# Performance work log

Measured on AMD Instinct MI355X. Metric: run time of the kernel, lower is better.

The kernel has to match this reference:

```python
import jax, jax.numpy as jnp
import numpy as np

B, N, D, K = 8, 2048, 512, 8192
DECAY = 0.99
COMMIT = 0.25
EPS = 1e-5


def setup_inputs() -> dict:
    key = jax.random.key(0)
    k1, k2 = jax.random.split(key, 2)
    encoded_latents = jax.random.normal(k1, (B, N, D), dtype=jnp.float32)
    embedding_weight = jax.random.normal(k2, (K, D), dtype=jnp.float32)
    # buffers: ema_codebook initialized as a clone of the embedding, sizes at zero
    ema_cluster_sizes = jnp.zeros((K,), dtype=jnp.float32)
    ema_codebook = embedding_weight
    return {
        "encoded_latents": encoded_latents,
        "embedding_weight": embedding_weight,
        "ema_cluster_sizes": ema_cluster_sizes,
        "ema_codebook": ema_codebook,
    }


def reference(encoded_latents, embedding_weight, ema_cluster_sizes, ema_codebook):
    # (B, N, D) -> (B*N, D)
    z = encoded_latents.reshape(-1, D)
    e = embedding_weight

    # ||z - e||^2 = z^2 - 2 z.e + e^2  via matmul  -> (B*N, K)
    z_sq = jnp.sum(z * z, axis=1, keepdims=True)
    e_sq = jnp.sum(e * e, axis=1)
    distances = z_sq - 2.0 * (z @ e.T) + e_sq

    nearest = jnp.argmin(distances, axis=-1)          # (B*N,)
    quantized_flat = e[nearest]                        # gather -> (B*N, D)

    # --- training-mode EMA codebook update (no-grad buffer math) ---
    z_ng = jax.lax.stop_gradient(z)
    cluster_sizes = jax.ops.segment_sum(
        jnp.ones(z.shape[0], dtype=jnp.float32), nearest, num_segments=K)
    weighted_sum = jax.ops.segment_sum(z_ng, nearest, num_segments=K)
    new_ema_cluster_sizes = ema_cluster_sizes * DECAY + cluster_sizes * (1.0 - DECAY)
    new_ema_codebook = ema_codebook * DECAY + weighted_sum * (1.0 - DECAY)
    new_embedding = new_ema_codebook / (new_ema_cluster_sizes[:, None] + EPS)

    quantized = quantized_flat.reshape(B, N, D)
    commitment_loss = COMMIT * jnp.mean(
        (encoded_latents - jax.lax.stop_gradient(quantized)) ** 2)

    # STE exactly as written in the torch module: grad flows into `quantized`
    quantized_ste = quantized + jax.lax.stop_gradient(encoded_latents - quantized)
    indices = nearest.reshape(B, N)
    return (quantized_ste, indices, commitment_loss,
            new_ema_cluster_sizes, new_ema_codebook, new_embedding)
```

## Files before the change

kernel.cpp:

```cpp
#include <hip/hip_runtime.h>
#include <cfloat>

#define B_SZ 8
#define N_SZ 2048
#define D_SZ 512
#define K_SZ 8192
#define M_SZ (B_SZ * N_SZ)

#define DECAY_F 0.99f
#define OMD_F ((float)(1.0 - 0.99))
#define EPS_F 1e-5f

#define OUT1_OFF 8388608
#define OUT2_OFF 8404992
#define OUT3_OFF 8404993
#define OUT4_OFF 8413185
#define OUT5_OFF 12607489

typedef unsigned short ushort_t;
typedef unsigned int uint_t;
typedef short bf16x8 __attribute__((ext_vector_type(8)));
typedef float f32x4 __attribute__((ext_vector_type(4)));

__device__ inline ushort_t f2bf(float v) {
    union { float f; uint_t u; } x; x.f = v;
    uint_t r = x.u + 0x7FFFu + ((x.u >> 16) & 1u);
    return (ushort_t)(r >> 16);
}

__device__ __forceinline__ void gl16(const void* g, void* l) {
    __builtin_amdgcn_global_load_lds(
        (const __attribute__((address_space(1))) uint_t*)g,
        (__attribute__((address_space(3))) uint_t*)l, 16, 0, 0);
}

__global__ __launch_bounds__(256) void k_esq(const float* __restrict__ e,
                                             float* __restrict__ esq) {
    int row = blockIdx.x * 4 + (threadIdx.x >> 6);
    int lane = threadIdx.x & 63;
    const float4* er = (const float4*)(e + (size_t)row * D_SZ);
    float s = 0.f;
#pragma unroll
    for (int i = 0; i < 2; ++i) {
        float4 v = er[lane + i * 64];
        s += v.x * v.x + v.y * v.y + v.z * v.z + v.w * v.w;
    }
#pragma unroll
    for (int off = 32; off; off >>= 1) s += __shfl_down(s, off);
    if (lane == 0) esq[row] = s;
}

__global__ __launch_bounds__(256) void k_split_e(const float* __restrict__ in,
                                                 ushort_t* __restrict__ ebuf) {
    int idx = blockIdx.x * 256 + threadIdx.x;
    int row = idx >> 6, o = idx & 63;
    int ch = o >> 3, kg = o & 7;
    const float* src = in + (size_t)row * D_SZ + o * 8;
    float4 a = *(const float4*)src;
    float4 b = *(const float4*)(src + 4);
    float vv[8] = {a.x, a.y, a.z, a.w, b.x, b.y, b.z, b.w};
    ushort_t o1[8];
#pragma unroll
    for (int j = 0; j < 8; ++j) o1[j] = f2bf(vv[j]);
    int cb = row >> 7, rl = row & 127;
    size_t base = (size_t)(cb * 8 + ch) * 16384 + rl * 128;
    *(uint4*)((unsigned char*)ebuf + base + ((kg ^ (rl & 7)) << 4)) = *(uint4*)o1;
}

__global__ __launch_bounds__(256) void k_split_z(const float* __restrict__ in,
                                                 ushort_t* __restrict__ zbuf) {
    int idx = blockIdx.x * 256 + threadIdx.x;
    int row = idx >> 6, o = idx & 63;
    int ch = o >> 3, kg = o & 7;
    const float* src = in + (size_t)row * D_SZ + o * 8;
    float4 a = *(const float4*)src;
    float4 b = *(const float4*)(src + 4);
    float vv[8] = {a.x, a.y, a.z, a.w, b.x, b.y, b.z, b.w};
    ushort_t o1[8];
#pragma unroll
    for (int j = 0; j < 8; ++j) o1[j] = f2bf(vv[j]);
    int zi = row >> 7, rl = row & 127;
    size_t base = (size_t)(zi * 8 + ch) * 16384 + rl * 128;
    *(uint4*)((unsigned char*)zbuf + base + ((kg ^ (rl & 7)) << 4)) = *(uint4*)o1;
}

__global__ __launch_bounds__(256) void k_init(const float* __restrict__ cb,
                                              const float* __restrict__ sizes,
                                              float* __restrict__ out3,
                                              float* __restrict__ out4) {
    int i = blockIdx.x * 256 + threadIdx.x;
    out4[i] = cb[i] * DECAY_F;
    if (i < K_SZ) out3[i] = sizes[i] * DECAY_F;
}

__global__ __launch_bounds__(256) void k_copy(const float* __restrict__ z,
                                              float* __restrict__ out0) {
    int i = blockIdx.x * 256 + threadIdx.x;
    ((float4*)out0)[i] = ((const float4*)z)[i];
}

__global__ __launch_bounds__(256) void k_scatter(const float* __restrict__ z,
                                                 const float* __restrict__ e,
                                                 const int* __restrict__ nearest,
                                                 float* __restrict__ out3,
                                                 float* __restrict__ out4,
                                                 float* __restrict__ lossAcc) {
    const int tid = threadIdx.x;
    float lp = 0.f;
    const int base_row = blockIdx.x * 8;
#pragma unroll
    for (int r = 0; r < 8; ++r) {
        int row = base_row + r;
        int n = nearest[row];
        float2 zv = ((const float2*)(z + (size_t)row * D_SZ))[tid];
        float2 ev = ((const float2*)(e + (size_t)n * D_SZ))[tid];
        float* o4 = out4 + (size_t)n * D_SZ + tid * 2;
        atomicAdd(o4, OMD_F * zv.x);
        atomicAdd(o4 + 1, OMD_F * zv.y);
        float dx = zv.x - ev.x, dy = zv.y - ev.y;
        lp += dx * dx + dy * dy;
        if (tid == 0) atomicAdd(out3 + n, OMD_F);
    }
#pragma unroll
    for (int off = 32; off; off >>= 1) lp += __shfl_down(lp, off);
    __shared__ float red[4];
    if ((tid & 63) == 0) red[tid >> 6] = lp;
    __syncthreads();
    if (tid == 0) atomicAdd(lossAcc, red[0] + red[1] + red[2] + red[3]);
}

__global__ __launch_bounds__(256) void k_final(const float* __restrict__ out3,
                                               const float* __restrict__ out4,
                                               float* __restrict__ out5,
                                               const float* __restrict__ lossAcc,
                                               float* __restrict__ out2) {
    int i = blockIdx.x * 256 + threadIdx.x;
    out5[i] = out4[i] / (out3[i >> 9] + EPS_F);
    if (i == 0) out2[0] = 0.25f * lossAcc[0] / 8388608.0f;
}

__global__ __launch_bounds__(512, 4) void k_pass1(const ushort_t* __restrict__ ebuf,
                                                  const ushort_t* __restrict__ zbuf,
                                                  const float* __restrict__ esq,
                                                  float* __restrict__ candD,
                                                  ushort_t* __restrict__ candI) {
    __shared__ __align__(16) unsigned char ldsb[65536];

    const int tid = threadIdx.x;
    const int lane = tid & 63;
    const int wv = tid >> 6;
    const int mw = wv >> 2;
    const int nw = wv & 3;
    const int lr = lane & 15;
    const int g = lane >> 4;

    const int xcd = blockIdx.x & 7;
    const int cbl = (blockIdx.x >> 3) & 7;
    const int zi = blockIdx.x >> 6;
    const int cb = xcd * 8 + cbl;

    const unsigned char* esrc = (const unsigned char*)ebuf + (size_t)cb * 131072 + tid * 16;
    const unsigned char* zsrc = (const unsigned char*)zbuf + (size_t)zi * 131072 + tid * 16;

#define ISSUE(c, b) do {                                                \
        const unsigned char* ep_ = esrc + (c) * 16384;                  \
        const unsigned char* zp_ = zsrc + (c) * 16384;                  \
        unsigned char* el_ = ldsb + (b) * 32768 + tid * 16;             \
        unsigned char* zl_ = el_ + 16384;                               \
        gl16(ep_, el_); gl16(ep_ + 8192, el_ + 8192);                   \
        gl16(zp_, zl_); gl16(zp_ + 8192, zl_ + 8192);                   \
    } while (0)

    f32x4 acc[4][2];
#pragma unroll
    for (int mf = 0; mf < 4; ++mf)
#pragma unroll
        for (int nf = 0; nf < 2; ++nf)
            acc[mf][nf] = (f32x4){0.f, 0.f, 0.f, 0.f};

    ISSUE(0, 0);
    asm volatile("s_waitcnt vmcnt(0)" ::: "memory");
    __builtin_amdgcn_s_barrier();
    asm volatile("" ::: "memory");

    int cur = 0;
    for (int ch = 0; ch < 8; ++ch) {
        if (ch < 7) {
            if (cur) ISSUE(ch + 1, 0); else ISSUE(ch + 1, 1);
        }

        const unsigned char* eb = ldsb + cur * 32768;
        const unsigned char* zp = eb + 16384;

#pragma unroll
        for (int ks = 0; ks < 2; ++ks) {
            bf16x8 zf[2];
#pragma unroll
            for (int nf = 0; nf < 2; ++nf) {
                int row = nw * 32 + nf * 16 + lr;
                int sl = (ks * 4 + g) ^ (row & 7);
                zf[nf] = *(const bf16x8*)(zp + row * 128 + (sl << 4));
            }
#pragma unroll
            for (int mf = 0; mf < 4; ++mf) {
                int row = mw * 64 + mf * 16 + lr;
                int sl = (ks * 4 + g) ^ (row & 7);
                bf16x8 ef = *(const bf16x8*)(eb + row * 128 + (sl << 4));
#pragma unroll
                for (int nf = 0; nf < 2; ++nf)
                    acc[mf][nf] = __builtin_amdgcn_mfma_f32_16x16x32_bf16(ef, zf[nf], acc[mf][nf], 0, 0, 0);
            }
        }
        asm volatile("s_waitcnt vmcnt(0)" ::: "memory");
        __builtin_amdgcn_s_barrier();
        asm volatile("" ::: "memory");
        cur ^= 1;
    }
#undef ISSUE

    float b1[2], b2[2];
    int i1[2], i2[2];
#pragma unroll
    for (int nf = 0; nf < 2; ++nf) {
        b1[nf] = FLT_MAX; b2[nf] = FLT_MAX;
        i1[nf] = 0x7fffffff; i2[nf] = 0x7fffffff;
    }
    const int code0 = cb * 128 + mw * 64;
#pragma unroll
    for (int mf = 0; mf < 4; ++mf)
#pragma unroll
        for (int r = 0; r < 4; ++r) {
            int code = code0 + mf * 16 + g * 4 + r;
            float eq = esq[code];
#pragma unroll
            for (int nf = 0; nf < 2; ++nf) {
                float d = fmaf(-2.f, acc[mf][nf][r], eq);
                if (d < b1[nf]) {
                    b2[nf] = b1[nf]; i2[nf] = i1[nf];
                    b1[nf] = d; i1[nf] = code;
                } else if (d < b2[nf]) {
                    b2[nf] = d; i2[nf] = code;
                }
            }
        }

#pragma unroll
    for (int off = 16; off <= 32; off <<= 1) {
#pragma unroll
        for (int nf = 0; nf < 2; ++nf) {
            float ob1 = __shfl_xor(b1[nf], off); int oi1 = __shfl_xor(i1[nf], off);
            float ob2 = __shfl_xor(b2[nf], off); int oi2 = __shfl_xor(i2[nf], off);
            bool tA = (b1[nf] < ob1) || (b1[nf] == ob1 && i1[nf] <= oi1);
            float n1 = tA ? b1[nf] : ob1; int ni1 = tA ? i1[nf] : oi1;
            float ca = tA ? b2[nf] : ob2; int cia = tA ? i2[nf] : oi2;
            float cbv = tA ? ob1 : b1[nf]; int cib = tA ? oi1 : i1[nf];
            bool t2 = (ca < cbv) || (ca == cbv && cia <= cib);
            b1[nf] = n1; i1[nf] = ni1;
            b2[nf] = t2 ? ca : cbv; i2[nf] = t2 ? cia : cib;
        }
    }

    __syncthreads();
    float* mD = (float*)ldsb;
    int* mI = (int*)(ldsb + 1024);
    if (mw == 1 && g == 0) {
#pragma unroll
        for (int nf = 0; nf < 2; ++nf) {
            int zr = nw * 32 + nf * 16 + lr;
            mD[zr * 2] = b1[nf]; mD[zr * 2 + 1] = b2[nf];
            mI[zr * 2] = i1[nf]; mI[zr * 2 + 1] = i2[nf];
        }
    }
    __syncthreads();
    if (mw == 0 && g == 0) {
#pragma unroll
        for (int nf = 0; nf < 2; ++nf) {
            int zr = nw * 32 + nf * 16 + lr;
            float ob1 = mD[zr * 2], ob2 = mD[zr * 2 + 1];
            int oi1 = mI[zr * 2], oi2 = mI[zr * 2 + 1];
            bool tA = (b1[nf] < ob1) || (b1[nf] == ob1 && i1[nf] <= oi1);
            float n1 = tA ? b1[nf] : ob1; int ni1 = tA ? i1[nf] : oi1;
            float ca = tA ? b2[nf] : ob2; int cia = tA ? i2[nf] : oi2;
            float cbv = tA ? ob1 : b1[nf]; int cib = tA ? oi1 : i1[nf];
            bool t2 = (ca < cbv) || (ca == cbv && cia <= cib);
            float n2 = t2 ? ca : cbv; int ni2 = t2 ? cia : cib;
            int row = zi * 128 + zr;
            size_t base = (size_t)row * 128 + cb * 2;
            candD[base] = n1; candD[base + 1] = n2;
            candI[base] = (ushort_t)ni1; candI[base + 1] = (ushort_t)ni2;
        }
    }
}

__global__ __launch_bounds__(256) void k_refine(const float* __restrict__ z,
                                                const float* __restrict__ e,
                                                const float* __restrict__ esq,
                                                const float* __restrict__ candD,
                                                const ushort_t* __restrict__ candI,
                                                int* __restrict__ nearest,
                                                float* __restrict__ out1) {
    const int lane = threadIdx.x & 63;
    const int row = blockIdx.x * 4 + (threadIdx.x >> 6);

    const float4* zr = (const float4*)(z + (size_t)row * D_SZ + lane * 8);
    float4 za = zr[0], zb = zr[1];
    float zsq = za.x * za.x + za.y * za.y + za.z * za.z + za.w * za.w +
                zb.x * zb.x + zb.y * zb.y + zb.z * zb.z + zb.w * zb.w;
#pragma unroll
    for (int off = 32; off; off >>= 1) zsq += __shfl_xor(zsq, off);

    float da = candD[(size_t)row * 128 + lane];
    int ia = candI[(size_t)row * 128 + lane];
    float db = candD[(size_t)row * 128 + 64 + lane];
    int ib = candI[(size_t)row * 128 + 64 + lane];

    float best = FLT_MAX;
    int bidx = 0x7fffffff;
#pragma unroll
    for (int c = 0; c < 8; ++c) {
        bool pa = (da < db) || (da == db && ia < ib);
        float md = pa ? da : db;
        int mi = pa ? ia : ib;
#pragma unroll
        for (int off = 32; off; off >>= 1) {
            float od = __shfl_xor(md, off); int oi = __shfl_xor(mi, off);
            if (od < md || (od == md && oi < mi)) { md = od; mi = oi; }
        }
        if (ia == mi) da = FLT_MAX;
        if (ib == mi) db = FLT_MAX;
        const float4* er = (const float4*)(e + (size_t)mi * D_SZ + lane * 8);
        float4 ea = er[0], eb = er[1];
        float dot = za.x * ea.x + za.y * ea.y + za.z * ea.z + za.w * ea.w +
                    zb.x * eb.x + zb.y * eb.y + zb.z * eb.z + zb.w * eb.w;
#pragma unroll
        for (int off = 32; off; off >>= 1) dot += __shfl_xor(dot, off);
        float dex = (zsq - 2.f * dot) + esq[mi];
        if (dex < best || (dex == best && mi < bidx)) { best = dex; bidx = mi; }
    }
    if (lane == 0) {
        nearest[row] = bidx;
        out1[row] = (float)bidx;
    }
}

extern "C" void kernel_launch(void* const* d_in, const int* in_sizes, int n_in,
                              void* d_out, int out_size, void* d_ws, size_t ws_size,
                              hipStream_t stream) {
    const float* z = (const float*)d_in[0];
    const float* ew = (const float*)d_in[1];
    const float* sizes = (const float*)d_in[2];
    const float* cb = (const float*)d_in[3];

    float* out = (float*)d_out;
    float* out0 = out;
    float* out1 = out + OUT1_OFF;
    float* out2 = out + OUT2_OFF;
    float* out3 = out + OUT3_OFF;
    float* out4 = out + OUT4_OFF;
    float* out5 = out + OUT5_OFF;

    int* nearest = (int*)d_ws;
    float* esq = (float*)d_ws + M_SZ;
    float* lossAcc = (float*)d_ws + M_SZ + K_SZ;

    ushort_t* zbuf = (ushort_t*)out0;
    unsigned char* s4 = (unsigned char*)out4 + 12;
    ushort_t* ebuf = (ushort_t*)s4;
    float* candD = (float*)(s4 + 8388608);
    ushort_t* candI = (ushort_t*)(s4 + 8388608 + 8388608);

    hipMemsetAsync(lossAcc, 0, sizeof(float), stream);

    k_esq<<<K_SZ / 4, 256, 0, stream>>>(ew, esq);
    k_split_z<<<(M_SZ * 64) / 256, 256, 0, stream>>>(z, zbuf);
    k_split_e<<<(K_SZ * 64) / 256, 256, 0, stream>>>(ew, ebuf);

    k_pass1<<<8192, 512, 0, stream>>>(ebuf, zbuf, esq, candD, candI);
    k_refine<<<M_SZ / 4, 256, 0, stream>>>(z, ew, esq, candD, candI, nearest, out1);

    k_init<<<(K_SZ * D_SZ) / 256, 256, 0, stream>>>(cb, sizes, out3, out4);
    k_copy<<<(M_SZ * D_SZ / 4) / 256, 256, 0, stream>>>(z, out0);
    k_scatter<<<M_SZ / 8, 256, 0, stream>>>(z, ew, nearest, out3, out4, lossAcc);
    k_final<<<(K_SZ * D_SZ) / 256, 256, 0, stream>>>(out3, out4, out5, lossAcc, out2);
}
```

Measured before the change: 336.1 us.

## Enlarge pass1 tiles to 256x256 with 1024-thread blocks and fuse esq into split_e

The distance GEMM block tile grows from 128 codes x 128 rows to 256 x 256, using 1024 threads and 128KB of LDS, with each wave holding a 4x4 set of MFMA accumulators. Operands are reused more per tile and the number of per-block candidate pairs halves, which shrinks the candD/candI buffers and the refine kernel's input. The codebook squared-norm computation is folded into the bf16 split kernel, removing one launch and one read of the codebook. In exchange, occupancy drops to at most one block per CU, register pressure rises, and the cross-wave candidate merge becomes longer. Refine still checks the top 8 candidates per row, but these now come from a pool of 64 instead of 128.

```diff
diff --git a/kernel.cpp b/kernel.cpp
--- a/kernel.cpp
+++ b/kernel.cpp
@@ -34,24 +34,9 @@
         (__attribute__((address_space(3))) uint_t*)l, 16, 0, 0);
 }
 
-__global__ __launch_bounds__(256) void k_esq(const float* __restrict__ e,
-                                             float* __restrict__ esq) {
-    int row = blockIdx.x * 4 + (threadIdx.x >> 6);
-    int lane = threadIdx.x & 63;
-    const float4* er = (const float4*)(e + (size_t)row * D_SZ);
-    float s = 0.f;
-#pragma unroll
-    for (int i = 0; i < 2; ++i) {
-        float4 v = er[lane + i * 64];
-        s += v.x * v.x + v.y * v.y + v.z * v.z + v.w * v.w;
-    }
-#pragma unroll
-    for (int off = 32; off; off >>= 1) s += __shfl_down(s, off);
-    if (lane == 0) esq[row] = s;
-}
-
 __global__ __launch_bounds__(256) void k_split_e(const float* __restrict__ in,
-                                                 ushort_t* __restrict__ ebuf) {
+                                                 ushort_t* __restrict__ ebuf,
+                                                 float* __restrict__ esq) {
     int idx = blockIdx.x * 256 + threadIdx.x;
     int row = idx >> 6, o = idx & 63;
     int ch = o >> 3, kg = o & 7;
@@ -60,11 +45,18 @@
     float4 b = *(const float4*)(src + 4);
     float vv[8] = {a.x, a.y, a.z, a.w, b.x, b.y, b.z, b.w};
     ushort_t o1[8];
-#pragma unroll
-    for (int j = 0; j < 8; ++j) o1[j] = f2bf(vv[j]);
-    int cb = row >> 7, rl = row & 127;
-    size_t base = (size_t)(cb * 8 + ch) * 16384 + rl * 128;
+    float s = 0.f;
+#pragma unroll
+    for (int j = 0; j < 8; ++j) {
+        o1[j] = f2bf(vv[j]);
+        s += vv[j] * vv[j];
+    }
+    int cb = row >> 8, rl = row & 255;
+    size_t base = (size_t)(cb * 8 + ch) * 32768 + rl * 128;
     *(uint4*)((unsigned char*)ebuf + base + ((kg ^ (rl & 7)) << 4)) = *(uint4*)o1;
+#pragma unroll
+    for (int off = 32; off; off >>= 1) s += __shfl_down(s, off);
+    if ((threadIdx.x & 63) == 0) esq[row] = s;
 }
 
 __global__ __launch_bounds__(256) void k_split_z(const float* __restrict__ in,
@@ -79,8 +71,8 @@
     ushort_t o1[8];
 #pragma unroll
     for (int j = 0; j < 8; ++j) o1[j] = f2bf(vv[j]);
-    int zi = row >> 7, rl = row & 127;
-    size_t base = (size_t)(zi * 8 + ch) * 16384 + rl * 128;
+    int zi = row >> 8, rl = row & 255;
+    size_t base = (size_t)(zi * 8 + ch) * 32768 + rl * 128;
     *(uint4*)((unsigned char*)zbuf + base + ((kg ^ (rl & 7)) << 4)) = *(uint4*)o1;
 }
 
@@ -139,12 +131,12 @@
     if (i == 0) out2[0] = 0.25f * lossAcc[0] / 8388608.0f;
 }
 
-__global__ __launch_bounds__(512, 4) void k_pass1(const ushort_t* __restrict__ ebuf,
-                                                  const ushort_t* __restrict__ zbuf,
-                                                  const float* __restrict__ esq,
-                                                  float* __restrict__ candD,
-                                                  ushort_t* __restrict__ candI) {
-    __shared__ __align__(16) unsigned char ldsb[65536];
+__global__ __launch_bounds__(1024) void k_pass1(const ushort_t* __restrict__ ebuf,
+                                                const ushort_t* __restrict__ zbuf,
+                                                const float* __restrict__ esq,
+                                                float* __restrict__ candD,
+                                                ushort_t* __restrict__ candI) {
+    __shared__ __align__(16) unsigned char ldsb[131072];
 
     const int tid = threadIdx.x;
     const int lane = tid & 63;
@@ -155,27 +147,27 @@
     const int g = lane >> 4;
 
     const int xcd = blockIdx.x & 7;
-    const int cbl = (blockIdx.x >> 3) & 7;
-    const int zi = blockIdx.x >> 6;
-    const int cb = xcd * 8 + cbl;
-
-    const unsigned char* esrc = (const unsigned char*)ebuf + (size_t)cb * 131072 + tid * 16;
-    const unsigned char* zsrc = (const unsigned char*)zbuf + (size_t)zi * 131072 + tid * 16;
+    const int cbl = (blockIdx.x >> 3) & 3;
+    const int zi = blockIdx.x >> 5;
+    const int cb = xcd * 4 + cbl;
+
+    const unsigned char* esrc = (const unsigned char*)ebuf + (size_t)cb * 262144 + tid * 16;
+    const unsigned char* zsrc = (const unsigned char*)zbuf + (size_t)zi * 262144 + tid * 16;
 
 #define ISSUE(c, b) do {                                                \
-        const unsigned char* ep_ = esrc + (c) * 16384;                  \
-        const unsigned char* zp_ = zsrc + (c) * 16384;                  \
-        unsigned char* el_ = ldsb + (b) * 32768 + tid * 16;             \
-        unsigned char* zl_ = el_ + 16384;                               \
-        gl16(ep_, el_); gl16(ep_ + 8192, el_ + 8192);                   \
-        gl16(zp_, zl_); gl16(zp_ + 8192, zl_ + 8192);                   \
+        const unsigned char* ep_ = esrc + (c) * 32768;                  \
+        const unsigned char* zp_ = zsrc + (c) * 32768;                  \
+        unsigned char* el_ = ldsb + (b) * 65536 + tid * 16;             \
+        unsigned char* zl_ = el_ + 32768;                               \
+        gl16(ep_, el_); gl16(ep_ + 16384, el_ + 16384);                 \
+        gl16(zp_, zl_); gl16(zp_ + 16384, zl_ + 16384);                 \
     } while (0)
 
-    f32x4 acc[4][2];
+    f32x4 acc[4][4];
 #pragma unroll
     for (int mf = 0; mf < 4; ++mf)
 #pragma unroll
-        for (int nf = 0; nf < 2; ++nf)
+        for (int nf = 0; nf < 4; ++nf)
             acc[mf][nf] = (f32x4){0.f, 0.f, 0.f, 0.f};
 
     ISSUE(0, 0);
@@ -189,15 +181,15 @@
             if (cur) ISSUE(ch + 1, 0); else ISSUE(ch + 1, 1);
         }
 
-        const unsigned char* eb = ldsb + cur * 32768;
-        const unsigned char* zp = eb + 16384;
+        const unsigned char* eb = ldsb + cur * 65536;
+        const unsigned char* zp = eb + 32768;
 
 #pragma unroll
         for (int ks = 0; ks < 2; ++ks) {
-            bf16x8 zf[2];
-#pragma unroll
-            for (int nf = 0; nf < 2; ++nf) {
-                int row = nw * 32 + nf * 16 + lr;
+            bf16x8 zf[4];
+#pragma unroll
+            for (int nf = 0; nf < 4; ++nf) {
+                int row = nw * 64 + nf * 16 + lr;
                 int sl = (ks * 4 + g) ^ (row & 7);
                 zf[nf] = *(const bf16x8*)(zp + row * 128 + (sl << 4));
             }
@@ -207,7 +199,7 @@
                 int sl = (ks * 4 + g) ^ (row & 7);
                 bf16x8 ef = *(const bf16x8*)(eb + row * 128 + (sl << 4));
 #pragma unroll
-                for (int nf = 0; nf < 2; ++nf)
+                for (int nf = 0; nf < 4; ++nf)
                     acc[mf][nf] = __builtin_amdgcn_mfma_f32_16x16x32_bf16(ef, zf[nf], acc[mf][nf], 0, 0, 0);
             }
         }
@@ -218,14 +210,14 @@
     }
 #undef ISSUE
 
-    float b1[2], b2[2];
-    int i1[2], i2[2];
-#pragma unroll
-    for (int nf = 0; nf < 2; ++nf) {
+    float b1[4], b2[4];
+    int i1[4], i2[4];
+#pragma unroll
+    for (int nf = 0; nf < 4; ++nf) {
         b1[nf] = FLT_MAX; b2[nf] = FLT_MAX;
         i1[nf] = 0x7fffffff; i2[nf] = 0x7fffffff;
     }
-    const int code0 = cb * 128 + mw * 64;
+    const int code0 = cb * 256 + mw * 64;
 #pragma unroll
     for (int mf = 0; mf < 4; ++mf)
 #pragma unroll
@@ -233,7 +225,7 @@
             int code = code0 + mf * 16 + g * 4 + r;
             float eq = esq[code];
 #pragma unroll
-            for (int nf = 0; nf < 2; ++nf) {
+            for (int nf = 0; nf < 4; ++nf) {
                 float d = fmaf(-2.f, acc[mf][nf][r], eq);
                 if (d < b1[nf]) {
                     b2[nf] = b1[nf]; i2[nf] = i1[nf];
@@ -247,7 +239,7 @@
 #pragma unroll
     for (int off = 16; off <= 32; off <<= 1) {
 #pragma unroll
-        for (int nf = 0; nf < 2; ++nf) {
+        for (int nf = 0; nf < 4; ++nf) {
             float ob1 = __shfl_xor(b1[nf], off); int oi1 = __shfl_xor(i1[nf], off);
             float ob2 = __shfl_xor(b2[nf], off); int oi2 = __shfl_xor(i2[nf], off);
             bool tA = (b1[nf] < ob1) || (b1[nf] == ob1 && i1[nf] <= oi1);
@@ -262,32 +254,38 @@
 
     __syncthreads();
     float* mD = (float*)ldsb;
-    int* mI = (int*)(ldsb + 1024);
-    if (mw == 1 && g == 0) {
-#pragma unroll
-        for (int nf = 0; nf < 2; ++nf) {
-            int zr = nw * 32 + nf * 16 + lr;
-            mD[zr * 2] = b1[nf]; mD[zr * 2 + 1] = b2[nf];
-            mI[zr * 2] = i1[nf]; mI[zr * 2 + 1] = i2[nf];
+    int* mI = (int*)(ldsb + 8192);
+    if (mw != 0 && g == 0) {
+#pragma unroll
+        for (int nf = 0; nf < 4; ++nf) {
+            int zr = nw * 64 + nf * 16 + lr;
+            int s = ((mw - 1) * 256 + zr) * 2;
+            mD[s] = b1[nf]; mD[s + 1] = b2[nf];
+            mI[s] = i1[nf]; mI[s + 1] = i2[nf];
         }
     }
     __syncthreads();
     if (mw == 0 && g == 0) {
 #pragma unroll
-        for (int nf = 0; nf < 2; ++nf) {
-            int zr = nw * 32 + nf * 16 + lr;
-            float ob1 = mD[zr * 2], ob2 = mD[zr * 2 + 1];
-            int oi1 = mI[zr * 2], oi2 = mI[zr * 2 + 1];
-            bool tA = (b1[nf] < ob1) || (b1[nf] == ob1 && i1[nf] <= oi1);
-            float n1 = tA ? b1[nf] : ob1; int ni1 = tA ? i1[nf] : oi1;
-            float ca = tA ? b2[nf] : ob2; int cia = tA ? i2[nf] : oi2;
-            float cbv = tA ? ob1 : b1[nf]; int cib = tA ? oi1 : i1[nf];
-            bool t2 = (ca < cbv) || (ca == cbv && cia <= cib);
-            float n2 = t2 ? ca : cbv; int ni2 = t2 ? cia : cib;
-            int row = zi * 128 + zr;
-            size_t base = (size_t)row * 128 + cb * 2;
-            candD[base] = n1; candD[base + 1] = n2;
-            candI[base] = (ushort_t)ni1; candI[base + 1] = (ushort_t)ni2;
+        for (int nf = 0; nf < 4; ++nf) {
+            int zr = nw * 64 + nf * 16 + lr;
+#pragma unroll
+            for (int p = 0; p < 3; ++p) {
+                int s = (p * 256 + zr) * 2;
+                float ob1 = mD[s], ob2 = mD[s + 1];
+                int oi1 = mI[s], oi2 = mI[s + 1];
+                bool tA = (b1[nf] < ob1) || (b1[nf] == ob1 && i1[nf] <= oi1);
+                float n1 = tA ? b1[nf] : ob1; int ni1 = tA ? i1[nf] : oi1;
+                float ca = tA ? b2[nf] : ob2; int cia = tA ? i2[nf] : oi2;
+                float cbv = tA ? ob1 : b1[nf]; int cib = tA ? oi1 : i1[nf];
+                bool t2 = (ca < cbv) || (ca == cbv && cia <= cib);
+                b1[nf] = n1; i1[nf] = ni1;
+                b2[nf] = t2 ? ca : cbv; i2[nf] = t2 ? cia : cib;
+            }
+            int row = zi * 256 + zr;
+            size_t base = (size_t)row * 64 + cb * 2;
+            candD[base] = b1[nf]; candD[base + 1] = b2[nf];
+            candI[base] = (ushort_t)i1[nf]; candI[base + 1] = (ushort_t)i2[nf];
         }
     }
 }
@@ -309,25 +307,21 @@
 #pragma unroll
     for (int off = 32; off; off >>= 1) zsq += __shfl_xor(zsq, off);
 
-    float da = candD[(size_t)row * 128 + lane];
-    int ia = candI[(size_t)row * 128 + lane];
-    float db = candD[(size_t)row * 128 + 64 + lane];
-    int ib = candI[(size_t)row * 128 + 64 + lane];
+    float da = candD[(size_t)row * 64 + lane];
+    int ia = candI[(size_t)row * 64 + lane];
 
     float best = FLT_MAX;
     int bidx = 0x7fffffff;
 #pragma unroll
     for (int c = 0; c < 8; ++c) {
-        bool pa = (da < db) || (da == db && ia < ib);
-        float md = pa ? da : db;
-        int mi = pa ? ia : ib;
+        float md = da;
+        int mi = ia;
 #pragma unroll
         for (int off = 32; off; off >>= 1) {
             float od = __shfl_xor(md, off); int oi = __shfl_xor(mi, off);
             if (od < md || (od == md && oi < mi)) { md = od; mi = oi; }
         }
         if (ia == mi) da = FLT_MAX;
-        if (ib == mi) db = FLT_MAX;
         const float4* er = (const float4*)(e + (size_t)mi * D_SZ + lane * 8);
         float4 ea = er[0], eb = er[1];
         float dot = za.x * ea.x + za.y * ea.y + za.z * ea.z + za.w * ea.w +
@@ -367,15 +361,14 @@
     unsigned char* s4 = (unsigned char*)out4 + 12;
     ushort_t* ebuf = (ushort_t*)s4;
     float* candD = (float*)(s4 + 8388608);
-    ushort_t* candI = (ushort_t*)(s4 + 8388608 + 8388608);
+    ushort_t* candI = (ushort_t*)(s4 + 8388608 + 4194304);
 
     hipMemsetAsync(lossAcc, 0, sizeof(float), stream);
 
-    k_esq<<<K_SZ / 4, 256, 0, stream>>>(ew, esq);
     k_split_z<<<(M_SZ * 64) / 256, 256, 0, stream>>>(z, zbuf);
-    k_split_e<<<(K_SZ * 64) / 256, 256, 0, stream>>>(ew, ebuf);
-
-    k_pass1<<<8192, 512, 0, stream>>>(ebuf, zbuf, esq, candD, candI);
+    k_split_e<<<(K_SZ * 64) / 256, 256, 0, stream>>>(ew, ebuf, esq);
+
+    k_pass1<<<2048, 1024, 0, stream>>>(ebuf, zbuf, esq, candD, candI);
     k_refine<<<M_SZ / 4, 256, 0, stream>>>(z, ew, esq, candD, candI, nearest, out1);
 
     k_init<<<(K_SZ * D_SZ) / 256, 256, 0, stream>>>(cb, sizes, out3, out4);
```

New measurement: 383.7 us. +14.2%, slower.

## Load z fragments directly from global into registers, halving LDS staging

Applied to the files above, without the earlier changes.

The z tile is no longer staged through LDS. Each lane reads its bf16 z fragments straight from global memory in an unswizzled layout, so k_split_z drops the XOR swizzle, and LDS shrinks to only the double-buffered codebook tiles. The aim is to cut LDS traffic and footprint and to raise occupancy, since the min-blocks launch bound is also removed. The cost is that the z loads become direct global loads issued at the start of each chunk and waited on by the same vmcnt(0), which may expose their latency instead of prefetching them.

```diff
diff --git a/kernel.cpp b/kernel.cpp
--- a/kernel.cpp
+++ b/kernel.cpp
@@ -81,7 +81,7 @@
     for (int j = 0; j < 8; ++j) o1[j] = f2bf(vv[j]);
     int zi = row >> 7, rl = row & 127;
     size_t base = (size_t)(zi * 8 + ch) * 16384 + rl * 128;
-    *(uint4*)((unsigned char*)zbuf + base + ((kg ^ (rl & 7)) << 4)) = *(uint4*)o1;
+    *(uint4*)((unsigned char*)zbuf + base + (kg << 4)) = *(uint4*)o1;
 }
 
 __global__ __launch_bounds__(256) void k_init(const float* __restrict__ cb,
@@ -139,12 +139,12 @@
     if (i == 0) out2[0] = 0.25f * lossAcc[0] / 8388608.0f;
 }
 
-__global__ __launch_bounds__(512, 4) void k_pass1(const ushort_t* __restrict__ ebuf,
-                                                  const ushort_t* __restrict__ zbuf,
-                                                  const float* __restrict__ esq,
-                                                  float* __restrict__ candD,
-                                                  ushort_t* __restrict__ candI) {
-    __shared__ __align__(16) unsigned char ldsb[65536];
+__global__ __launch_bounds__(512) void k_pass1(const ushort_t* __restrict__ ebuf,
+                                               const ushort_t* __restrict__ zbuf,
+                                               const float* __restrict__ esq,
+                                               float* __restrict__ candD,
+                                               ushort_t* __restrict__ candI) {
+    __shared__ __align__(16) unsigned char ldsb[32768];
 
     const int tid = threadIdx.x;
     const int lane = tid & 63;
@@ -160,15 +160,13 @@
     const int cb = xcd * 8 + cbl;
 
     const unsigned char* esrc = (const unsigned char*)ebuf + (size_t)cb * 131072 + tid * 16;
-    const unsigned char* zsrc = (const unsigned char*)zbuf + (size_t)zi * 131072 + tid * 16;
+    const unsigned char* zlane = (const unsigned char*)zbuf + (size_t)zi * 131072
+                                 + (nw * 32 + lr) * 128 + (g << 4);
 
 #define ISSUE(c, b) do {                                                \
         const unsigned char* ep_ = esrc + (c) * 16384;                  \
-        const unsigned char* zp_ = zsrc + (c) * 16384;                  \
-        unsigned char* el_ = ldsb + (b) * 32768 + tid * 16;             \
-        unsigned char* zl_ = el_ + 16384;                               \
+        unsigned char* el_ = ldsb + (b) * 16384 + tid * 16;             \
         gl16(ep_, el_); gl16(ep_ + 8192, el_ + 8192);                   \
-        gl16(zp_, zl_); gl16(zp_ + 8192, zl_ + 8192);                   \
     } while (0)
 
     f32x4 acc[4][2];
@@ -185,30 +183,29 @@
 
     int cur = 0;
     for (int ch = 0; ch < 8; ++ch) {
+        const unsigned char* zp = zlane + ch * 16384;
+        bf16x8 zv00 = *(const bf16x8*)(zp);
+        bf16x8 zv01 = *(const bf16x8*)(zp + 64);
+        bf16x8 zv10 = *(const bf16x8*)(zp + 2048);
+        bf16x8 zv11 = *(const bf16x8*)(zp + 2048 + 64);
+
         if (ch < 7) {
             if (cur) ISSUE(ch + 1, 0); else ISSUE(ch + 1, 1);
         }
 
-        const unsigned char* eb = ldsb + cur * 32768;
-        const unsigned char* zp = eb + 16384;
+        const unsigned char* eb = ldsb + cur * 16384;
 
 #pragma unroll
         for (int ks = 0; ks < 2; ++ks) {
-            bf16x8 zf[2];
-#pragma unroll
-            for (int nf = 0; nf < 2; ++nf) {
-                int row = nw * 32 + nf * 16 + lr;
-                int sl = (ks * 4 + g) ^ (row & 7);
-                zf[nf] = *(const bf16x8*)(zp + row * 128 + (sl << 4));
-            }
+            bf16x8 zf0 = ks ? zv01 : zv00;
+            bf16x8 zf1 = ks ? zv11 : zv10;
 #pragma unroll
             for (int mf = 0; mf < 4; ++mf) {
                 int row = mw * 64 + mf * 16 + lr;
                 int sl = (ks * 4 + g) ^ (row & 7);
                 bf16x8 ef = *(const bf16x8*)(eb + row * 128 + (sl << 4));
-#pragma unroll
-                for (int nf = 0; nf < 2; ++nf)
-                    acc[mf][nf] = __builtin_amdgcn_mfma_f32_16x16x32_bf16(ef, zf[nf], acc[mf][nf], 0, 0, 0);
+                acc[mf][0] = __builtin_amdgcn_mfma_f32_16x16x32_bf16(ef, zf0, acc[mf][0], 0, 0, 0);
+                acc[mf][1] = __builtin_amdgcn_mfma_f32_16x16x32_bf16(ef, zf1, acc[mf][1], 0, 0, 0);
             }
         }
         asm volatile("s_waitcnt vmcnt(0)" ::: "memory");
```

Measured after the change: 456.6 us. 35.8% more time.
